# Kernel tuning notes

Hardware: AMD Instinct MI355X
Metric: run time of the kernel (lower is better)

Reference implementation:

```python
import jax, jax.numpy as jnp
import numpy as np

D_MODEL = 1024
N_HEADS = 16
D_K = D_MODEL // N_HEADS
SEQ = 2048
BATCH = 2
THETA = 10000.0


def _rope(x, token_positions):
    # x: [b, h, s, dk]; token_positions: [s] int
    k = jnp.arange(0, D_K, 2, dtype=jnp.float32)
    freqs = 1.0 / (THETA ** (k / D_K))                    # [dk/2]
    angles = token_positions.astype(jnp.float32)[:, None] * freqs[None, :]  # [s, dk/2]
    cos = jnp.cos(angles)
    sin = jnp.sin(angles)
    x1 = x[..., 0::2]
    x2 = x[..., 1::2]
    r1 = x1 * cos - x2 * sin
    r2 = x1 * sin + x2 * cos
    out = jnp.stack([r1, r2], axis=-1)                    # [b,h,s,dk/2,2]
    return out.reshape(x.shape)


def setup_inputs() -> dict:
    key = jax.random.key(0)
    ks = jax.random.split(key, 5)
    sigma = np.sqrt(2.0 / (D_MODEL + D_MODEL))
    x = jax.random.normal(ks[0], (BATCH, SEQ, D_MODEL), dtype=jnp.float32)
    Wq = jax.random.truncated_normal(ks[1], -3.0, 3.0, (D_MODEL, D_MODEL), dtype=jnp.float32) * sigma
    Wk = jax.random.truncated_normal(ks[2], -3.0, 3.0, (D_MODEL, D_MODEL), dtype=jnp.float32) * sigma
    Wv = jax.random.truncated_normal(ks[3], -3.0, 3.0, (D_MODEL, D_MODEL), dtype=jnp.float32) * sigma
    Wo = jax.random.truncated_normal(ks[4], -3.0, 3.0, (D_MODEL, D_MODEL), dtype=jnp.float32) * sigma
    token_positions = jnp.arange(SEQ, dtype=jnp.int64)
    return {"x": x, "Wq": Wq, "Wk": Wk, "Wv": Wv, "Wo": Wo, "token_positions": token_positions}


def reference(x, Wq, Wk, Wv, Wo, token_positions):
    b, s, d = x.shape
    # projections: Linear stores weight [out,in], applies x @ W.T
    Q = x @ Wq.T
    K = x @ Wk.T
    V = x @ Wv.T
    # [b, s, h*dk] -> [b, h, s, dk]
    def split_heads(t):
        return t.reshape(b, s, N_HEADS, D_K).transpose(0, 2, 1, 3)
    Q, K, V = split_heads(Q), split_heads(K), split_heads(V)
    Q = _rope(Q, token_positions)
    K = _rope(K, token_positions)
    scale = 1.0 / np.sqrt(D_K).astype(np.float32)
    scores = jnp.einsum('bhqd,bhkd->bhqk', Q, K) * scale   # [b,h,s,s]
    causal = jnp.tril(jnp.ones((s, s), dtype=bool))
    scores = jnp.where(causal, scores, -jnp.inf)
    attn = jax.nn.softmax(scores, axis=-1)
    out = jnp.einsum('bhqk,bhkd->bhqd', attn, V)           # [b,h,s,dk]
    out = out.transpose(0, 2, 1, 3).reshape(b, s, d)
    return out @ Wo.T
```

## Files before the change

kernel.cpp:

```cpp
#include <hip/hip_runtime.h>
#include <hip/hip_bf16.h>
#include <stdint.h>

#define SEQL   2048
#define NBATCH 2
#define BSZ    4096
#define DMODEL 1024
#define NH     16
#define DK     64
#define NBH    32
#define NCHUNK_TOT 40

typedef __attribute__((ext_vector_type(8)))  short short8;
typedef __attribute__((ext_vector_type(4)))  short shortx4;
typedef __attribute__((ext_vector_type(4)))  float f32x4;
typedef __attribute__((ext_vector_type(16))) float f32x16;
typedef __attribute__((ext_vector_type(4)))  unsigned uint4v;
union PU { uint4v u; short8 s; };

__device__ __forceinline__ short f2b(float f) {
  unsigned u = __float_as_uint(f);
  u = (u + 0x7FFF + ((u >> 16) & 1)) >> 16;
  return (short)u;
}
__device__ __forceinline__ float b2f(short s) {
  return __uint_as_float(((unsigned)(unsigned short)s) << 16);
}
__device__ __forceinline__ unsigned cvtpk(float lo, float hi) {
  unsigned r;
  asm("v_cvt_pk_bf16_f32 %0, %1, %2" : "=v"(r) : "v"(lo), "v"(hi));
  return r;
}
#define PLSWAP(a_, b_) asm("v_permlane32_swap_b32 %0, %1" : "+v"(a_), "+v"(b_))

__device__ __forceinline__ void g2l16(const void* g, void* l) {
  __builtin_amdgcn_global_load_lds(
      (__attribute__((address_space(1))) void*)(uintptr_t)g,
      (__attribute__((address_space(3))) void*)l, 16, 0, 0);
}

__device__ __forceinline__ f32x4 mfma16(short8 a, short8 b, f32x4 c) {
  return __builtin_amdgcn_mfma_f32_16x16x32_bf16(a, b, c, 0, 0, 0);
}
__device__ __forceinline__ f32x16 mfma32(short8 a, short8 b, f32x16 c) {
  return __builtin_amdgcn_mfma_f32_32x32x16_bf16(a, b, c, 0, 0, 0);
}

__global__ void cvt_all(const float* __restrict__ x,  const float* __restrict__ wq,
                        const float* __restrict__ wk, const float* __restrict__ wv,
                        const float* __restrict__ wo, short* __restrict__ xb,
                        short* __restrict__ wqkv, short* __restrict__ wob) {
  long idx = ((long)blockIdx.x * 256 + threadIdx.x) * 4;
  const float* s; short* d; long off;
  if (idx < 4194304L)      { s = x;  d = xb;             off = idx; }
  else if (idx < 5242880L) { s = wq; d = wqkv;           off = idx - 4194304L; }
  else if (idx < 6291456L) { s = wk; d = wqkv + 1048576; off = idx - 5242880L; }
  else if (idx < 7340032L) { s = wv; d = wqkv + 2097152; off = idx - 6291456L; }
  else                     { s = wo; d = wob;            off = idx - 7340032L; }
  float4 v = *(const float4*)(s + off);
  shortx4 r;
  r[0] = f2b(v.x); r[1] = f2b(v.y); r[2] = f2b(v.z); r[3] = f2b(v.w);
  *(shortx4*)(d + off) = r;
}

template<int CBF16>
__global__ __launch_bounds__(256, 2)
void gemm_bt(const short* __restrict__ A, const short* __restrict__ B,
             void* __restrict__ Cv, int M, int N, int K,
             long bStride, long cStride) {
  __shared__ short As[4096];
  __shared__ short Bs[4096];
  B += (long)blockIdx.y * bStride;
  int nbn = N >> 7;
  int bm = blockIdx.x / nbn, bn = blockIdx.x % nbn;
  int tid = threadIdx.x, w = tid >> 6, l = tid & 63;
  int wm = w >> 1, wn = w & 1;
  int lr = l & 15, lg = l >> 4;
  int brow = bm << 7, bcol = bn << 7;

  const f32x4 fz = {0.f, 0.f, 0.f, 0.f};
  f32x4 acc[4][4];
#pragma unroll
  for (int xi = 0; xi < 4; ++xi)
#pragma unroll
    for (int yi = 0; yi < 4; ++yi) acc[xi][yi] = fz;

  for (int k0 = 0; k0 < K; k0 += 32) {
#pragma unroll
    for (int i = 0; i < 2; ++i) {
      int c = w * 2 + i;
      int chunk = c * 64 + l;
      int row = chunk >> 2, ch = chunk & 3;
      int gch = ch ^ ((row >> 1) & 3);
      g2l16(A + (long)(brow + row) * K + k0 + gch * 8, &As[c * 512]);
      g2l16(B + (long)(bcol + row) * K + k0 + gch * 8, &Bs[c * 512]);
    }
    __syncthreads();

    short8 af[4], bf[4];
#pragma unroll
    for (int xi = 0; xi < 4; ++xi) {
      int ar = wm * 64 + xi * 16 + lr;
      af[xi] = *(const short8*)&As[ar * 32 + ((lg ^ ((ar >> 1) & 3)) << 3)];
      int br = wn * 64 + xi * 16 + lr;
      bf[xi] = *(const short8*)&Bs[br * 32 + ((lg ^ ((br >> 1) & 3)) << 3)];
    }
#pragma unroll
    for (int xi = 0; xi < 4; ++xi)
#pragma unroll
      for (int yi = 0; yi < 4; ++yi)
        acc[xi][yi] = mfma16(af[xi], bf[yi], acc[xi][yi]);
    __syncthreads();
  }

  if (CBF16) {
    short* C = (short*)Cv + (long)blockIdx.y * cStride;
#pragma unroll
    for (int xi = 0; xi < 4; ++xi)
#pragma unroll
      for (int yi = 0; yi < 4; ++yi)
#pragma unroll
        for (int r = 0; r < 4; ++r) {
          int row = brow + wm * 64 + xi * 16 + lg * 4 + r;
          int col = bcol + wn * 64 + yi * 16 + lr;
          C[(long)row * N + col] = f2b(acc[xi][yi][r]);
        }
  } else {
    float* C = (float*)Cv;
#pragma unroll
    for (int xi = 0; xi < 4; ++xi)
#pragma unroll
      for (int yi = 0; yi < 4; ++yi)
#pragma unroll
        for (int r = 0; r < 4; ++r) {
          int row = brow + wm * 64 + xi * 16 + lg * 4 + r;
          int col = bcol + wn * 64 + yi * 16 + lr;
          C[(long)row * N + col] = acc[xi][yi][r];
        }
  }
}

__global__ void rope_split(const short* __restrict__ qkv, const int* __restrict__ tok,
                           short* __restrict__ Qh, short* __restrict__ Kh) {
  int t = blockIdx.x * 256 + threadIdx.x;
  int qd = t & 15, h = (t >> 4) & 15, bs = t >> 8;
  int b = bs >> 11, s = bs & 2047;
  float pos = (float)tok[s];
  long srcoff = (long)bs * 1024 + h * 64 + qd * 4;
  shortx4 q4 = *(const shortx4*)(qkv + srcoff);
  shortx4 k4 = *(const shortx4*)(qkv + 4194304L + srcoff);
  shortx4 qo, ko;
#pragma unroll
  for (int p = 0; p < 2; ++p) {
    int i = qd * 2 + p;
    float freq = exp2f(-(float)i * (13.287712379549449f / 32.0f));
    float ang = pos * freq;
    float sn, cs;
    sincosf(ang, &sn, &cs);
    const float QS = 0.125f * 1.44269504f;
    float x1 = b2f(q4[p * 2]), x2 = b2f(q4[p * 2 + 1]);
    qo[p * 2]     = f2b((x1 * cs - x2 * sn) * QS);
    qo[p * 2 + 1] = f2b((x1 * sn + x2 * cs) * QS);
    float y1 = b2f(k4[p * 2]), y2 = b2f(k4[p * 2 + 1]);
    ko[p * 2]     = f2b(y1 * cs - y2 * sn);
    ko[p * 2 + 1] = f2b(y1 * sn + y2 * cs);
  }
  long outoff = ((long)(b * 16 + h) * 2048 + s) * 64 + qd * 4;
  *(shortx4*)(Qh + outoff) = qo;
  *(shortx4*)(Kh + outoff) = ko;
}

__global__ void vtrans(const short* __restrict__ Vlin, short* __restrict__ Vt) {
  __shared__ short tile[64][72];
  int s0 = blockIdx.x * 64;
  int bh = blockIdx.y;
  int b = bh >> 4, h = bh & 15;
  int t = threadIdx.x;
  int r = t >> 2, c0 = (t & 3) * 16;
  const short* src = Vlin + ((long)(b * 2048 + s0 + r)) * 1024 + h * 64 + c0;
  *(short8*)&tile[r][c0]     = *(const short8*)src;
  *(short8*)&tile[r][c0 + 8] = *(const short8*)(src + 8);
  __syncthreads();
  int d = t >> 2, sc0 = (t & 3) * 16;
  short8 o0, o1;
#pragma unroll
  for (int j = 0; j < 8; ++j) { o0[j] = tile[sc0 + j][d]; o1[j] = tile[sc0 + 8 + j][d]; }
  short* dst = Vt + ((long)(bh * 64 + d)) * 2048 + s0 + sc0;
  *(short8*)dst       = o0;
  *(short8*)(dst + 8) = o1;
}

__global__ __launch_bounds__(256, 3)
void attn_fwd(const short* __restrict__ Qh, const short* __restrict__ Kh,
              const short* __restrict__ Vt, short* __restrict__ poO,
              float* __restrict__ pmb, float* __restrict__ plb) {
  __shared__ short Ks[3][4096];
  __shared__ short Vs[3][4096];
  int bh = blockIdx.x;
  int xr = 39 - blockIdx.y;
  int qi, c = xr, nc = 1;
  for (qi = 0; qi < 16; ++qi) { nc = (qi >> 2) + 1; if (c < nc) break; c -= nc; }
  int n = 2 * qi + 2;
  int t0 = (c * n) / nc, t1 = ((c + 1) * n) / nc;
  int q0b = qi << 7;
  int tid = threadIdx.x, w = tid >> 6, l = tid & 63;
  int ql = l & 31, hi = l >> 5;
  const short* Qb = Qh + (long)bh * (2048 * 64);
  const short* Kb = Kh + (long)bh * (2048 * 64);
  const short* Vb = Vt + (long)bh * (64 * 2048);
  int qw = q0b + 32 * w;
  int qg = qw + ql;
  int pid = bh * NCHUNK_TOT + xr;

  short8 qf[4];
#pragma unroll
  for (int kc = 0; kc < 4; ++kc)
    qf[kc] = *(const short8*)(Qb + (long)qg * 64 + kc * 16 + hi * 8);

  f32x16 o0, o1;
#pragma unroll
  for (int r = 0; r < 16; ++r) { o0[r] = 0.f; o1[r] = 0.f; }
  float m = -1e30f, lsum = 0.f;

#define STAGE(t_, bufi_) do {                                                   \
    int s0_ = (t_) << 6;                                                        \
    _Pragma("unroll")                                                           \
    for (int i_ = 0; i_ < 2; ++i_) {                                            \
      int c_ = w + 4 * i_;                                                      \
      int g_ = c_ >> 2, cc_ = c_ & 3;                                           \
      g2l16(Kb + ((long)(s0_ + g_ * 32 + ql)) * 64 + cc_ * 16 + hi * 8,         \
            &Ks[bufi_][c_ * 512]);                                              \
      g2l16(Vb + ((long)(g_ * 32 + ql)) * 2048 + s0_ + cc_ * 16 + hi * 8,       \
            &Vs[bufi_][c_ * 512]);                                              \
    }                                                                           \
  } while (0)

  STAGE(t0, 0);
  if (t0 + 1 < t1) STAGE(t0 + 1, 1);
  int cur = 0;

  for (int t = t0; t < t1; ++t) {
    if (t + 2 < t1) {
      int nb = cur + 2; if (nb >= 3) nb -= 3;
      STAGE(t + 2, nb);
      asm volatile("s_waitcnt vmcnt(8)" ::: "memory");
    } else if (t + 1 < t1) {
      asm volatile("s_waitcnt vmcnt(4)" ::: "memory");
    } else {
      asm volatile("s_waitcnt vmcnt(0)" ::: "memory");
    }
    __builtin_amdgcn_s_barrier();
    int s0 = t << 6;
    if (s0 <= qw + 31) {
      bool upper = (s0 + 32 <= qw + 31);
      f32x16 sT0, sT1;
#pragma unroll
      for (int r = 0; r < 16; ++r) { sT0[r] = 0.f; sT1[r] = 0.f; }
      __builtin_amdgcn_s_setprio(1);
#pragma unroll
      for (int kc = 0; kc < 4; ++kc) {
        short8 k0 = *(const short8*)&Ks[cur][(kc * 64 + l) * 8];
        sT0 = mfma32(k0, qf[kc], sT0);
      }
      if (upper) {
#pragma unroll
        for (int kc = 0; kc < 4; ++kc) {
          short8 k1 = *(const short8*)&Ks[cur][((4 + kc) * 64 + l) * 8];
          sT1 = mfma32(k1, qf[kc], sT1);
        }
      }
      __builtin_amdgcn_s_setprio(0);
      if (s0 + 63 > qw) {
#pragma unroll
        for (int r = 0; r < 16; ++r) {
          int kvl = (r & 3) + 8 * (r >> 2) + 4 * hi;
          if (s0 + kvl > qg) sT0[r] = -1e30f;
        }
        if (upper) {
#pragma unroll
          for (int r = 0; r < 16; ++r) {
            int kvl = (r & 3) + 8 * (r >> 2) + 4 * hi;
            if (s0 + 32 + kvl > qg) sT1[r] = -1e30f;
          }
        }
      }
      float pmax = sT0[0];
#pragma unroll
      for (int r = 1; r < 16; ++r) pmax = fmaxf(pmax, sT0[r]);
      if (upper) {
#pragma unroll
        for (int r = 0; r < 16; ++r) pmax = fmaxf(pmax, sT1[r]);
      }
      pmax = fmaxf(pmax, __shfl_xor(pmax, 32));
      if (__any(pmax > m + 11.5416f)) {
        float mn = fmaxf(m, pmax);
        float sf = exp2f(m - mn);
        m = mn;
        lsum *= sf;
#pragma unroll
        for (int r = 0; r < 16; ++r) {
          int row = (r & 3) + 8 * (r >> 2) + 4 * hi;
          float fo = __shfl(sf, row);
          o0[r] *= fo; o1[r] *= fo;
        }
      }
      float rs = 0.f;
#pragma unroll
      for (int r = 0; r < 16; ++r) {
        float p = exp2f(sT0[r] - m);
        sT0[r] = p; rs += p;
      }
      if (upper) {
#pragma unroll
        for (int r = 0; r < 16; ++r) {
          float p = exp2f(sT1[r] - m);
          sT1[r] = p; rs += p;
        }
      }
      rs += __shfl_xor(rs, 32);
      lsum += rs;
      short8 pa[4];
      {
        unsigned cA[4], cB[4];
#pragma unroll
        for (int g = 0; g < 4; ++g) {
          cA[g] = cvtpk(sT0[4 * g], sT0[4 * g + 1]);
          cB[g] = cvtpk(sT0[4 * g + 2], sT0[4 * g + 3]);
        }
        PLSWAP(cA[0], cA[1]); PLSWAP(cB[0], cB[1]);
        PLSWAP(cA[2], cA[3]); PLSWAP(cB[2], cB[3]);
        PU p0; p0.u = (uint4v){cA[0], cB[0], cA[1], cB[1]}; pa[0] = p0.s;
        PU p1; p1.u = (uint4v){cA[2], cB[2], cA[3], cB[3]}; pa[1] = p1.s;
      }
      if (upper) {
        unsigned cA[4], cB[4];
#pragma unroll
        for (int g = 0; g < 4; ++g) {
          cA[g] = cvtpk(sT1[4 * g], sT1[4 * g + 1]);
          cB[g] = cvtpk(sT1[4 * g + 2], sT1[4 * g + 3]);
        }
        PLSWAP(cA[0], cA[1]); PLSWAP(cB[0], cB[1]);
        PLSWAP(cA[2], cA[3]); PLSWAP(cB[2], cB[3]);
        PU p2; p2.u = (uint4v){cA[0], cB[0], cA[1], cB[1]}; pa[2] = p2.s;
        PU p3; p3.u = (uint4v){cA[2], cB[2], cA[3], cB[3]}; pa[3] = p3.s;
      }
      __builtin_amdgcn_s_setprio(1);
#pragma unroll
      for (int kc = 0; kc < 2; ++kc) {
        short8 v0 = *(const short8*)&Vs[cur][(kc * 64 + l) * 8];
        short8 v1 = *(const short8*)&Vs[cur][((4 + kc) * 64 + l) * 8];
        o0 = mfma32(pa[kc], v0, o0);
        o1 = mfma32(pa[kc], v1, o1);
      }
      if (upper) {
#pragma unroll
        for (int kc = 2; kc < 4; ++kc) {
          short8 v0 = *(const short8*)&Vs[cur][(kc * 64 + l) * 8];
          short8 v1 = *(const short8*)&Vs[cur][((4 + kc) * 64 + l) * 8];
          o0 = mfma32(pa[kc], v0, o0);
          o1 = mfma32(pa[kc], v1, o1);
        }
      }
      __builtin_amdgcn_s_setprio(0);
    }
    asm volatile("s_waitcnt lgkmcnt(0)" ::: "memory");
    __builtin_amdgcn_s_barrier();
    ++cur; if (cur >= 3) cur -= 3;
  }
#undef STAGE

  if (hi == 0) {
    pmb[pid * 128 + w * 32 + ql] = m;
    plb[pid * 128 + w * 32 + ql] = lsum;
  }
#pragma unroll
  for (int r = 0; r < 16; ++r) {
    int row = (r & 3) + 8 * (r >> 2) + 4 * hi;
    long basep = ((long)pid * 128 + w * 32 + row) * 64;
    poO[basep + ql]      = f2b(o0[r]);
    poO[basep + 32 + ql] = f2b(o1[r]);
  }
}

__global__ void attn_combine(const short* __restrict__ poO,
                             const float* __restrict__ pmb,
                             const float* __restrict__ plb,
                             short* __restrict__ Oh) {
  int x = blockIdx.x, bh = blockIdx.y;
  int qi = x >> 2, sub = x & 3;
  int t = threadIdx.x;
  int r = sub * 32 + (t >> 3);
  int d0 = (t & 7) * 8;
  int nc = (qi >> 2) + 1;
  int prefix = 0;
  for (int j = 0; j < qi; ++j) prefix += (j >> 2) + 1;
  int base = bh * NCHUNK_TOT + prefix;
  float M = -1e30f;
  for (int i = 0; i < nc; ++i)
    M = fmaxf(M, pmb[(base + i) * 128 + r]);
  float acc0 = 0, acc1 = 0, acc2 = 0, acc3 = 0, acc4 = 0, acc5 = 0, acc6 = 0, acc7 = 0;
  float den = 0.f;
  for (int i = 0; i < nc; ++i) {
    float wgt = exp2f(pmb[(base + i) * 128 + r] - M);
    den += wgt * plb[(base + i) * 128 + r];
    short8 ov = *(const short8*)&poO[((long)(base + i) * 128 + r) * 64 + d0];
    acc0 += wgt * b2f(ov[0]); acc1 += wgt * b2f(ov[1]);
    acc2 += wgt * b2f(ov[2]); acc3 += wgt * b2f(ov[3]);
    acc4 += wgt * b2f(ov[4]); acc5 += wgt * b2f(ov[5]);
    acc6 += wgt * b2f(ov[6]); acc7 += wgt * b2f(ov[7]);
  }
  float inv = 1.0f / den;
  int b = bh >> 4, h = bh & 15;
  int s = qi * 128 + r;
  short8 out;
  out[0] = f2b(acc0 * inv); out[1] = f2b(acc1 * inv);
  out[2] = f2b(acc2 * inv); out[3] = f2b(acc3 * inv);
  out[4] = f2b(acc4 * inv); out[5] = f2b(acc5 * inv);
  out[6] = f2b(acc6 * inv); out[7] = f2b(acc7 * inv);
  *(short8*)&Oh[((long)(b * 2048 + s)) * 1024 + h * 64 + d0] = out;
}

extern "C" void kernel_launch(void* const* d_in, const int* in_sizes, int n_in,
                              void* d_out, int out_size, void* d_ws, size_t ws_size,
                              hipStream_t stream) {
  const float* x  = (const float*)d_in[0];
  const float* wq = (const float*)d_in[1];
  const float* wk = (const float*)d_in[2];
  const float* wv = (const float*)d_in[3];
  const float* wo = (const float*)d_in[4];
  const int* tok  = (const int*)d_in[5];

  short* wsp  = (short*)d_ws;
  short* xb   = wsp;
  short* wqkv = xb + 4194304;
  short* wob  = wqkv + 3145728;
  short* qkv  = wob + 1048576;
  short* qh   = qkv + 12582912;
  short* kh   = qh + 4194304;
  short* vt   = kh + 4194304;
  short* oh   = vt + 4194304;

  short* poO = qkv;
  float* pmb = (float*)xb;
  float* plb = pmb + NCHUNK_TOT * NBH * 128;

  (void)in_sizes; (void)n_in; (void)out_size; (void)ws_size;

  cvt_all<<<8192, 256, 0, stream>>>(x, wq, wk, wv, wo, xb, wqkv, wob);
  gemm_bt<1><<<dim3(256, 3), 256, 0, stream>>>(xb, wqkv, qkv, 4096, 1024, 1024,
                                               1048576L, 4194304L);
  rope_split<<<4096, 256, 0, stream>>>(qkv, tok, qh, kh);
  vtrans<<<dim3(32, 32), 256, 0, stream>>>(qkv + 8388608, vt);
  attn_fwd<<<dim3(32, NCHUNK_TOT), 256, 0, stream>>>(qh, kh, vt, poO, pmb, plb);
  attn_combine<<<dim3(64, 32), 256, 0, stream>>>(poO, pmb, plb, oh);
  gemm_bt<0><<<dim3(256, 1), 256, 0, stream>>>(oh, wob, d_out, 4096, 1024, 1024,
                                               0L, 0L);
}
```

Measured before the change: 130.5 us.

## Double-buffer GEMM LDS tiles and split attention into single-wave blocks

The GEMM now double-buffers its A/B LDS tiles, prefetching the next K-slice while the current one is computed, with explicit vmcnt waits and MFMA priority boosting. Separately, the attention kernel drops shared-memory K/V staging: each 64-thread block (one wave) loads K and V fragments straight from global memory into registers, and the grid has four times as many blocks. This removes block-wide barriers and LDS usage and lets waves that finish early exit. The cost is that the four waves working on the same query tile no longer share K/V tiles, so global and cache traffic goes up and loads are not prefetched ahead of the math.

```diff
diff --git a/kernel.cpp b/kernel.cpp
--- a/kernel.cpp
+++ b/kernel.cpp
@@ -68,8 +68,8 @@
 void gemm_bt(const short* __restrict__ A, const short* __restrict__ B,
              void* __restrict__ Cv, int M, int N, int K,
              long bStride, long cStride) {
-  __shared__ short As[4096];
-  __shared__ short Bs[4096];
+  __shared__ short As[2][4096];
+  __shared__ short Bs[2][4096];
   B += (long)blockIdx.y * bStride;
   int nbn = N >> 7;
   int bm = blockIdx.x / nbn, bn = blockIdx.x % nbn;
@@ -85,33 +85,48 @@
 #pragma unroll
     for (int yi = 0; yi < 4; ++yi) acc[xi][yi] = fz;
 
+#define GSTAGE(k0_, bi_) do {                                                   \
+    _Pragma("unroll")                                                           \
+    for (int i_ = 0; i_ < 2; ++i_) {                                            \
+      int c_ = w * 2 + i_;                                                      \
+      int chunk_ = c_ * 64 + l;                                                 \
+      int row_ = chunk_ >> 2, ch_ = chunk_ & 3;                                 \
+      int gch_ = ch_ ^ ((row_ >> 1) & 3);                                       \
+      g2l16(A + (long)(brow + row_) * K + (k0_) + gch_ * 8, &As[bi_][c_ * 512]);\
+      g2l16(B + (long)(bcol + row_) * K + (k0_) + gch_ * 8, &Bs[bi_][c_ * 512]);\
+    }                                                                           \
+  } while (0)
+
+  GSTAGE(0, 0);
   for (int k0 = 0; k0 < K; k0 += 32) {
-#pragma unroll
-    for (int i = 0; i < 2; ++i) {
-      int c = w * 2 + i;
-      int chunk = c * 64 + l;
-      int row = chunk >> 2, ch = chunk & 3;
-      int gch = ch ^ ((row >> 1) & 3);
-      g2l16(A + (long)(brow + row) * K + k0 + gch * 8, &As[c * 512]);
-      g2l16(B + (long)(bcol + row) * K + k0 + gch * 8, &Bs[c * 512]);
-    }
-    __syncthreads();
+    int cb = (k0 >> 5) & 1;
+    if (k0 + 32 < K) {
+      GSTAGE(k0 + 32, cb ^ 1);
+      asm volatile("s_waitcnt vmcnt(4)" ::: "memory");
+    } else {
+      asm volatile("s_waitcnt vmcnt(0)" ::: "memory");
+    }
+    __builtin_amdgcn_s_barrier();
 
     short8 af[4], bf[4];
 #pragma unroll
     for (int xi = 0; xi < 4; ++xi) {
       int ar = wm * 64 + xi * 16 + lr;
-      af[xi] = *(const short8*)&As[ar * 32 + ((lg ^ ((ar >> 1) & 3)) << 3)];
+      af[xi] = *(const short8*)&As[cb][ar * 32 + ((lg ^ ((ar >> 1) & 3)) << 3)];
       int br = wn * 64 + xi * 16 + lr;
-      bf[xi] = *(const short8*)&Bs[br * 32 + ((lg ^ ((br >> 1) & 3)) << 3)];
-    }
+      bf[xi] = *(const short8*)&Bs[cb][br * 32 + ((lg ^ ((br >> 1) & 3)) << 3)];
+    }
+    __builtin_amdgcn_s_setprio(1);
 #pragma unroll
     for (int xi = 0; xi < 4; ++xi)
 #pragma unroll
       for (int yi = 0; yi < 4; ++yi)
         acc[xi][yi] = mfma16(af[xi], bf[yi], acc[xi][yi]);
-    __syncthreads();
-  }
+    __builtin_amdgcn_s_setprio(0);
+    asm volatile("s_waitcnt lgkmcnt(0)" ::: "memory");
+    __builtin_amdgcn_s_barrier();
+  }
+#undef GSTAGE
 
   if (CBF16) {
     short* C = (short*)Cv + (long)blockIdx.y * cStride;
@@ -190,20 +205,20 @@
   *(short8*)(dst + 8) = o1;
 }
 
-__global__ __launch_bounds__(256, 3)
+__global__ __launch_bounds__(64, 3)
 void attn_fwd(const short* __restrict__ Qh, const short* __restrict__ Kh,
               const short* __restrict__ Vt, short* __restrict__ poO,
               float* __restrict__ pmb, float* __restrict__ plb) {
-  __shared__ short Ks[3][4096];
-  __shared__ short Vs[3][4096];
   int bh = blockIdx.x;
-  int xr = 39 - blockIdx.y;
+  int y = blockIdx.y;
+  int xr = 39 - (y >> 2);
+  int w = y & 3;
   int qi, c = xr, nc = 1;
   for (qi = 0; qi < 16; ++qi) { nc = (qi >> 2) + 1; if (c < nc) break; c -= nc; }
   int n = 2 * qi + 2;
   int t0 = (c * n) / nc, t1 = ((c + 1) * n) / nc;
   int q0b = qi << 7;
-  int tid = threadIdx.x, w = tid >> 6, l = tid & 63;
+  int l = threadIdx.x;
   int ql = l & 31, hi = l >> 5;
   const short* Qb = Qh + (long)bh * (2048 * 64);
   const short* Kb = Kh + (long)bh * (2048 * 64);
@@ -222,152 +237,123 @@
   for (int r = 0; r < 16; ++r) { o0[r] = 0.f; o1[r] = 0.f; }
   float m = -1e30f, lsum = 0.f;
 
-#define STAGE(t_, bufi_) do {                                                   \
-    int s0_ = (t_) << 6;                                                        \
-    _Pragma("unroll")                                                           \
-    for (int i_ = 0; i_ < 2; ++i_) {                                            \
-      int c_ = w + 4 * i_;                                                      \
-      int g_ = c_ >> 2, cc_ = c_ & 3;                                           \
-      g2l16(Kb + ((long)(s0_ + g_ * 32 + ql)) * 64 + cc_ * 16 + hi * 8,         \
-            &Ks[bufi_][c_ * 512]);                                              \
-      g2l16(Vb + ((long)(g_ * 32 + ql)) * 2048 + s0_ + cc_ * 16 + hi * 8,       \
-            &Vs[bufi_][c_ * 512]);                                              \
-    }                                                                           \
-  } while (0)
-
-  STAGE(t0, 0);
-  if (t0 + 1 < t1) STAGE(t0 + 1, 1);
-  int cur = 0;
-
   for (int t = t0; t < t1; ++t) {
-    if (t + 2 < t1) {
-      int nb = cur + 2; if (nb >= 3) nb -= 3;
-      STAGE(t + 2, nb);
-      asm volatile("s_waitcnt vmcnt(8)" ::: "memory");
-    } else if (t + 1 < t1) {
-      asm volatile("s_waitcnt vmcnt(4)" ::: "memory");
-    } else {
-      asm volatile("s_waitcnt vmcnt(0)" ::: "memory");
-    }
-    __builtin_amdgcn_s_barrier();
     int s0 = t << 6;
-    if (s0 <= qw + 31) {
-      bool upper = (s0 + 32 <= qw + 31);
-      f32x16 sT0, sT1;
-#pragma unroll
-      for (int r = 0; r < 16; ++r) { sT0[r] = 0.f; sT1[r] = 0.f; }
-      __builtin_amdgcn_s_setprio(1);
-#pragma unroll
-      for (int kc = 0; kc < 4; ++kc) {
-        short8 k0 = *(const short8*)&Ks[cur][(kc * 64 + l) * 8];
-        sT0 = mfma32(k0, qf[kc], sT0);
+    if (s0 > qw + 31) break;
+    bool upper = (s0 + 32 <= qw + 31);
+    const short* kb = Kb + (long)s0 * 64;
+    short8 klo[4], khi[4];
+#pragma unroll
+    for (int kc = 0; kc < 4; ++kc)
+      klo[kc] = *(const short8*)(kb + ql * 64 + kc * 16 + hi * 8);
+    if (upper) {
+#pragma unroll
+      for (int kc = 0; kc < 4; ++kc)
+        khi[kc] = *(const short8*)(kb + (32 + ql) * 64 + kc * 16 + hi * 8);
+    }
+    f32x16 sT0, sT1;
+#pragma unroll
+    for (int r = 0; r < 16; ++r) { sT0[r] = 0.f; sT1[r] = 0.f; }
+#pragma unroll
+    for (int kc = 0; kc < 4; ++kc) sT0 = mfma32(klo[kc], qf[kc], sT0);
+    if (upper) {
+#pragma unroll
+      for (int kc = 0; kc < 4; ++kc) sT1 = mfma32(khi[kc], qf[kc], sT1);
+    }
+    const short* vb = Vb + s0;
+    short8 vlo[4], vhi[4];
+#pragma unroll
+    for (int kc = 0; kc < 4; ++kc) {
+      vlo[kc] = *(const short8*)(vb + ql * 2048 + kc * 16 + hi * 8);
+      vhi[kc] = *(const short8*)(vb + (32 + ql) * 2048 + kc * 16 + hi * 8);
+    }
+    if (s0 + 63 > qw) {
+#pragma unroll
+      for (int r = 0; r < 16; ++r) {
+        int kvl = (r & 3) + 8 * (r >> 2) + 4 * hi;
+        if (s0 + kvl > qg) sT0[r] = -1e30f;
       }
       if (upper) {
-#pragma unroll
-        for (int kc = 0; kc < 4; ++kc) {
-          short8 k1 = *(const short8*)&Ks[cur][((4 + kc) * 64 + l) * 8];
-          sT1 = mfma32(k1, qf[kc], sT1);
-        }
-      }
-      __builtin_amdgcn_s_setprio(0);
-      if (s0 + 63 > qw) {
 #pragma unroll
         for (int r = 0; r < 16; ++r) {
           int kvl = (r & 3) + 8 * (r >> 2) + 4 * hi;
-          if (s0 + kvl > qg) sT0[r] = -1e30f;
+          if (s0 + 32 + kvl > qg) sT1[r] = -1e30f;
         }
-        if (upper) {
-#pragma unroll
-          for (int r = 0; r < 16; ++r) {
-            int kvl = (r & 3) + 8 * (r >> 2) + 4 * hi;
-            if (s0 + 32 + kvl > qg) sT1[r] = -1e30f;
-          }
-        }
-      }
-      float pmax = sT0[0];
-#pragma unroll
-      for (int r = 1; r < 16; ++r) pmax = fmaxf(pmax, sT0[r]);
-      if (upper) {
-#pragma unroll
-        for (int r = 0; r < 16; ++r) pmax = fmaxf(pmax, sT1[r]);
-      }
-      pmax = fmaxf(pmax, __shfl_xor(pmax, 32));
-      if (__any(pmax > m + 11.5416f)) {
-        float mn = fmaxf(m, pmax);
-        float sf = exp2f(m - mn);
-        m = mn;
-        lsum *= sf;
-#pragma unroll
-        for (int r = 0; r < 16; ++r) {
-          int row = (r & 3) + 8 * (r >> 2) + 4 * hi;
-          float fo = __shfl(sf, row);
-          o0[r] *= fo; o1[r] *= fo;
-        }
-      }
-      float rs = 0.f;
+      }
+    }
+    float pmax = sT0[0];
+#pragma unroll
+    for (int r = 1; r < 16; ++r) pmax = fmaxf(pmax, sT0[r]);
+    if (upper) {
+#pragma unroll
+      for (int r = 0; r < 16; ++r) pmax = fmaxf(pmax, sT1[r]);
+    }
+    pmax = fmaxf(pmax, __shfl_xor(pmax, 32));
+    if (__any(pmax > m + 11.5416f)) {
+      float mn = fmaxf(m, pmax);
+      float sf = exp2f(m - mn);
+      m = mn;
+      lsum *= sf;
 #pragma unroll
       for (int r = 0; r < 16; ++r) {
-        float p = exp2f(sT0[r] - m);
-        sT0[r] = p; rs += p;
-      }
-      if (upper) {
-#pragma unroll
-        for (int r = 0; r < 16; ++r) {
-          float p = exp2f(sT1[r] - m);
-          sT1[r] = p; rs += p;
-        }
-      }
-      rs += __shfl_xor(rs, 32);
-      lsum += rs;
-      short8 pa[4];
-      {
-        unsigned cA[4], cB[4];
-#pragma unroll
-        for (int g = 0; g < 4; ++g) {
-          cA[g] = cvtpk(sT0[4 * g], sT0[4 * g + 1]);
-          cB[g] = cvtpk(sT0[4 * g + 2], sT0[4 * g + 3]);
-        }
-        PLSWAP(cA[0], cA[1]); PLSWAP(cB[0], cB[1]);
-        PLSWAP(cA[2], cA[3]); PLSWAP(cB[2], cB[3]);
-        PU p0; p0.u = (uint4v){cA[0], cB[0], cA[1], cB[1]}; pa[0] = p0.s;
-        PU p1; p1.u = (uint4v){cA[2], cB[2], cA[3], cB[3]}; pa[1] = p1.s;
-      }
-      if (upper) {
-        unsigned cA[4], cB[4];
-#pragma unroll
-        for (int g = 0; g < 4; ++g) {
-          cA[g] = cvtpk(sT1[4 * g], sT1[4 * g + 1]);
-          cB[g] = cvtpk(sT1[4 * g + 2], sT1[4 * g + 3]);
-        }
-        PLSWAP(cA[0], cA[1]); PLSWAP(cB[0], cB[1]);
-        PLSWAP(cA[2], cA[3]); PLSWAP(cB[2], cB[3]);
-        PU p2; p2.u = (uint4v){cA[0], cB[0], cA[1], cB[1]}; pa[2] = p2.s;
-        PU p3; p3.u = (uint4v){cA[2], cB[2], cA[3], cB[3]}; pa[3] = p3.s;
-      }
-      __builtin_amdgcn_s_setprio(1);
-#pragma unroll
-      for (int kc = 0; kc < 2; ++kc) {
-        short8 v0 = *(const short8*)&Vs[cur][(kc * 64 + l) * 8];
-        short8 v1 = *(const short8*)&Vs[cur][((4 + kc) * 64 + l) * 8];
-        o0 = mfma32(pa[kc], v0, o0);
-        o1 = mfma32(pa[kc], v1, o1);
-      }
-      if (upper) {
-#pragma unroll
-        for (int kc = 2; kc < 4; ++kc) {
-          short8 v0 = *(const short8*)&Vs[cur][(kc * 64 + l) * 8];
-          short8 v1 = *(const short8*)&Vs[cur][((4 + kc) * 64 + l) * 8];
-          o0 = mfma32(pa[kc], v0, o0);
-          o1 = mfma32(pa[kc], v1, o1);
-        }
-      }
-      __builtin_amdgcn_s_setprio(0);
-    }
-    asm volatile("s_waitcnt lgkmcnt(0)" ::: "memory");
-    __builtin_amdgcn_s_barrier();
-    ++cur; if (cur >= 3) cur -= 3;
-  }
-#undef STAGE
+        int row = (r & 3) + 8 * (r >> 2) + 4 * hi;
+        float fo = __shfl(sf, row);
+        o0[r] *= fo; o1[r] *= fo;
+      }
+    }
+    float rs = 0.f;
+#pragma unroll
+    for (int r = 0; r < 16; ++r) {
+      float p = exp2f(sT0[r] - m);
+      sT0[r] = p; rs += p;
+    }
+    if (upper) {
+#pragma unroll
+      for (int r = 0; r < 16; ++r) {
+        float p = exp2f(sT1[r] - m);
+        sT1[r] = p; rs += p;
+      }
+    }
+    rs += __shfl_xor(rs, 32);
+    lsum += rs;
+    short8 pa[4];
+    {
+      unsigned cA[4], cB[4];
+#pragma unroll
+      for (int g = 0; g < 4; ++g) {
+        cA[g] = cvtpk(sT0[4 * g], sT0[4 * g + 1]);
+        cB[g] = cvtpk(sT0[4 * g + 2], sT0[4 * g + 3]);
+      }
+      PLSWAP(cA[0], cA[1]); PLSWAP(cB[0], cB[1]);
+      PLSWAP(cA[2], cA[3]); PLSWAP(cB[2], cB[3]);
+      PU p0; p0.u = (uint4v){cA[0], cB[0], cA[1], cB[1]}; pa[0] = p0.s;
+      PU p1; p1.u = (uint4v){cA[2], cB[2], cA[3], cB[3]}; pa[1] = p1.s;
+    }
+    if (upper) {
+      unsigned cA[4], cB[4];
+#pragma unroll
+      for (int g = 0; g < 4; ++g) {
+        cA[g] = cvtpk(sT1[4 * g], sT1[4 * g + 1]);
+        cB[g] = cvtpk(sT1[4 * g + 2], sT1[4 * g + 3]);
+      }
+      PLSWAP(cA[0], cA[1]); PLSWAP(cB[0], cB[1]);
+      PLSWAP(cA[2], cA[3]); PLSWAP(cB[2], cB[3]);
+      PU p2; p2.u = (uint4v){cA[0], cB[0], cA[1], cB[1]}; pa[2] = p2.s;
+      PU p3; p3.u = (uint4v){cA[2], cB[2], cA[3], cB[3]}; pa[3] = p3.s;
+    }
+#pragma unroll
+    for (int kc = 0; kc < 2; ++kc) {
+      o0 = mfma32(pa[kc], vlo[kc], o0);
+      o1 = mfma32(pa[kc], vhi[kc], o1);
+    }
+    if (upper) {
+#pragma unroll
+      for (int kc = 2; kc < 4; ++kc) {
+        o0 = mfma32(pa[kc], vlo[kc], o0);
+        o1 = mfma32(pa[kc], vhi[kc], o1);
+      }
+    }
+  }
 
   if (hi == 0) {
     pmb[pid * 128 + w * 32 + ql] = m;
@@ -451,7 +437,7 @@
                                                1048576L, 4194304L);
   rope_split<<<4096, 256, 0, stream>>>(qkv, tok, qh, kh);
   vtrans<<<dim3(32, 32), 256, 0, stream>>>(qkv + 8388608, vt);
-  attn_fwd<<<dim3(32, NCHUNK_TOT), 256, 0, stream>>>(qh, kh, vt, poO, pmb, plb);
+  attn_fwd<<<dim3(32, 160), 64, 0, stream>>>(qh, kh, vt, poO, pmb, plb);
   attn_combine<<<dim3(64, 32), 256, 0, stream>>>(poO, pmb, plb, oh);
   gemm_bt<0><<<dim3(256, 1), 256, 0, stream>>>(oh, wob, d_out, 4096, 1024, 1024,
                                                0L, 0L);
```

Measured after the change: 163.2 us. 1.25x slower.
